# Optimization experiments

Measured on AMD Instinct MI355X. Metric: run time of the kernel, lower is better.

## Reference

```python
import jax, jax.numpy as jnp
import numpy as np

G, N, E, D, K = 32, 512, 8192, 256, 2048
LAMB_EDGE = 1.0
LAMB_NODE = 0.0
CODEBOOK_WEIGHT = 1000.0
ALPHA = 100.0


def setup_inputs() -> dict:
    key = jax.random.key(0)
    ks = jax.random.split(key, 12)
    s = 1.0 / np.sqrt(D)
    return {
        'feats': jax.random.normal(ks[0], (G, N, D), jnp.float32),
        'src': jax.random.randint(ks[1], (G, E), 0, N, jnp.int32),
        'dst': jax.random.randint(ks[2], (G, E), 0, N, jnp.int32),
        'W1': jax.random.normal(ks[3], (D, D), jnp.float32) * s,
        'b1': jnp.zeros((D,), jnp.float32),
        'W2': jax.random.normal(ks[4], (D, D), jnp.float32) * s,
        'b2': jnp.zeros((D,), jnp.float32),
        'ln_gamma': jnp.ones((D,), jnp.float32),
        'ln_beta': jnp.zeros((D,), jnp.float32),
        'dec1_W': jax.random.normal(ks[5], (D, D), jnp.float32) * s,
        'dec1_b': jnp.zeros((D,), jnp.float32),
        'dec2_W': jax.random.normal(ks[6], (D, D), jnp.float32) * s,
        'dec2_b': jnp.zeros((D,), jnp.float32),
        'codebook': jax.random.normal(ks[7], (K, D), jnp.float32),
    }


def _graph_conv(x, src, dst, W, b):
    # DGL GraphConv, norm='both': D_out^{-1/2} -> sum aggregate -> D_in^{-1/2} -> linear -> relu
    ones_e = jnp.ones(src.shape[0], x.dtype)
    deg_out = jnp.clip(jax.ops.segment_sum(ones_e, src, num_segments=N), 1.0)
    deg_in = jnp.clip(jax.ops.segment_sum(ones_e, dst, num_segments=N), 1.0)
    h = x * jax.lax.rsqrt(deg_out)[:, None]
    m = jax.ops.segment_sum(h[src], dst, num_segments=N)
    m = m * jax.lax.rsqrt(deg_in)[:, None]
    return jax.nn.relu(m @ W + b)


def _layernorm(x, gamma, beta):
    mu = jnp.mean(x, axis=-1, keepdims=True)
    var = jnp.mean(jnp.square(x - mu), axis=-1, keepdims=True)
    return (x - mu) * jax.lax.rsqrt(var + 1e-5) * gamma + beta


def _edge_loss(qe, src, dst):
    # qe: [N, D] decoded node embeddings for one graph
    logits = qe @ qe.T  # [N, N]
    adj = jnp.zeros((N, N), qe.dtype).at[src, dst].set(1.0)
    mask = jnp.triu(jnp.ones((N, N), bool), k=1)
    num_possible = N * N / 2.0
    num_edges = jnp.sum(jnp.where(mask, adj, 0.0))
    pos_weight = (num_possible - num_edges) / (num_edges + 1e-6)
    # BCEWithLogits with pos_weight, mean over strict upper triangle
    per = pos_weight * adj * jax.nn.softplus(-logits) + (1.0 - adj) * jax.nn.softplus(logits)
    return jnp.sum(jnp.where(mask, per, 0.0)) / (N * (N - 1) / 2.0)


def reference(feats, src, dst, W1, b1, W2, b2, ln_gamma, ln_beta,
              dec1_W, dec1_b, dec2_W, dec2_b, codebook):
    conv = jax.vmap(_graph_conv, in_axes=(0, 0, 0, None, None))
    h1 = conv(feats, src, dst, W1, b1)              # [G, N, D]
    h1 = _layernorm(h1, ln_gamma, ln_beta)           # dropout eval = identity
    h2 = conv(h1, src, dst, W2, b2)                  # [G, N, D]

    hf = h2.reshape(G * N, D)
    # cosine-sim VQ
    xn = hf * jax.lax.rsqrt(jnp.sum(hf * hf, -1, keepdims=True) + 1e-12)
    cn = codebook * jax.lax.rsqrt(jnp.sum(codebook * codebook, -1, keepdims=True) + 1e-12)
    dist = xn @ cn.T                                 # [G*N, K] cosine similarities
    idx = jnp.argmax(dist, axis=-1)
    q = codebook[idx]
    q_st = hf + jax.lax.stop_gradient(q - hf)        # straight-through
    vq_loss = CODEBOOK_WEIGHT * jnp.mean(jnp.square(q - jax.lax.stop_gradient(hf)))

    quantized_edge = (q_st @ dec1_W + dec1_b).reshape(G, N, D)
    quantized_node = q_st @ dec2_W + dec2_b

    edge_losses = jax.vmap(_edge_loss)(quantized_edge, src, dst)  # [G]
    edge_rec_loss = LAMB_EDGE * jnp.mean(edge_losses)
    feature_rec_loss = LAMB_NODE * jnp.mean(jnp.square(hf - quantized_node))
    loss = feature_rec_loss + edge_rec_loss * ALPHA + vq_loss
    return loss
```

## Files before the change

### kernel.cpp

```cpp
#include <hip/hip_runtime.h>
#include <math.h>

#define G 32
#define N 512
#define E 8192
#define D 256
#define KCB 2048
#define GN (G * N)

typedef __bf16 bf16x8 __attribute__((ext_vector_type(8)));
typedef float f32x4 __attribute__((ext_vector_type(4)));

static const size_t OFF_SPOS    = 0;
static const size_t OFF_SNEG    = OFF_SPOS + 256;
static const size_t OFF_NEDGE   = OFF_SNEG + 256;
static const size_t OFF_BEST    = OFF_NEDGE + 256;
static const size_t OFF_DEG_OUT = OFF_BEST + (size_t)GN * 8;
static const size_t OFF_DEG_IN  = OFF_DEG_OUT + (size_t)GN * 4;
static const size_t OFF_CURSOR  = OFF_DEG_IN + (size_t)GN * 4;
static const size_t OFF_ADJ     = OFF_CURSOR + (size_t)GN * 4;
static const size_t ZERO_BYTES  = OFF_ADJ + (size_t)G * N * N / 8;
static const size_t OFF_VQPART  = ZERO_BYTES;
static const size_t OFF_ROWOFF  = OFF_VQPART + (size_t)GN * 4;
static const size_t OFF_RS_OUT  = OFF_ROWOFF + (size_t)GN * 4;
static const size_t OFF_RS_IN   = OFF_RS_OUT + (size_t)GN * 4;
static const size_t OFF_CSR     = OFF_RS_IN + (size_t)GN * 4;
static const size_t OFF_RNC     = OFF_CSR + (size_t)G * E * 4;
static const size_t OFF_W1T     = OFF_RNC + (size_t)KCB * 4;
static const size_t OFF_W2T     = OFF_W1T + (size_t)D * D * 2;
static const size_t OFF_DWT     = OFF_W2T + (size_t)D * D * 2;
static const size_t OFF_CBB     = OFF_DWT + (size_t)D * D * 2;
static const size_t OFF_AGGB    = OFF_CBB + (size_t)KCB * D * 2;
static const size_t OFF_BF32    = OFF_AGGB + (size_t)GN * D * 2;
static const size_t OFF_BCB     = OFF_BF32 + (size_t)GN * D * 4;

__global__ void __launch_bounds__(256) k_build_deg(
    const int* __restrict__ src, const int* __restrict__ dst,
    int* __restrict__ deg_out, int* __restrict__ deg_in,
    unsigned* __restrict__ adj, int* __restrict__ nedge) {
  int b = blockIdx.x;
  int g = b >> 3;
  int e0 = (b & 7) << 10;
  int t = threadIdx.x;
  const int* sg = src + g * E;
  const int* dg = dst + g * E;
  int ecount = 0;
#pragma unroll
  for (int j = 0; j < 4; ++j) {
    int idx = e0 + j * 256 + t;
    int s = sg[idx], d = dg[idx];
    atomicAdd(&deg_out[(g << 9) | s], 1);
    atomicAdd(&deg_in[(g << 9) | d], 1);
    if (s < d) {
      int bit = s * N + d;
      unsigned m = 1u << (bit & 31);
      unsigned old = atomicOr(&adj[g * (N * N / 32) + (bit >> 5)], m);
      if (!(old & m)) ++ecount;
    }
  }
  for (int off = 32; off; off >>= 1) ecount += __shfl_down(ecount, off);
  __shared__ int sred[4];
  if ((t & 63) == 0) sred[t >> 6] = ecount;
  __syncthreads();
  if (t == 0) atomicAdd(&nedge[g], sred[0] + sred[1] + sred[2] + sred[3]);
}

__global__ void __launch_bounds__(512) k_build_scan(
    const int* __restrict__ deg_in, const int* __restrict__ deg_out,
    int* __restrict__ row_off, float* __restrict__ rs_in, float* __restrict__ rs_out) {
  int g = blockIdx.x, t = threadIdx.x;
  __shared__ int buf[2][N];
  int own = deg_in[(g << 9) | t];
  buf[0][t] = own;
  __syncthreads();
  int cur = 0;
  for (int off = 1; off < N; off <<= 1) {
    int v = buf[cur][t];
    if (t >= off) v += buf[cur][t - off];
    buf[cur ^ 1][t] = v;
    __syncthreads();
    cur ^= 1;
  }
  row_off[(g << 9) | t] = buf[cur][t] - own;
  rs_in[(g << 9) | t] = rsqrtf(fmaxf((float)own, 1.0f));
  rs_out[(g << 9) | t] = rsqrtf(fmaxf((float)deg_out[(g << 9) | t], 1.0f));
}

__global__ void __launch_bounds__(256) k_build_scatter(
    const int* __restrict__ src, const int* __restrict__ dst,
    const int* __restrict__ row_off, int* __restrict__ cursor, int* __restrict__ csr_src) {
  int b = blockIdx.x;
  int g = b >> 3;
  int e0 = (b & 7) << 10;
  int t = threadIdx.x;
  const int* sg = src + g * E;
  const int* dg = dst + g * E;
#pragma unroll
  for (int j = 0; j < 4; ++j) {
    int idx = e0 + j * 256 + t;
    int s = sg[idx], d = dg[idx];
    int gn = (g << 9) | d;
    int slot = atomicAdd(&cursor[gn], 1);
    csr_src[g * E + row_off[gn] + slot] = s;
  }
}

__global__ void __launch_bounds__(256) k_prep(
    const float* __restrict__ W1, const float* __restrict__ W2,
    const float* __restrict__ dW, __bf16* __restrict__ W1t,
    __bf16* __restrict__ W2t, __bf16* __restrict__ dWt,
    const float* __restrict__ cb, __bf16* __restrict__ cbb, float* __restrict__ rnc) {
  int b = blockIdx.x;
  if (b < 192) {
    __shared__ float tile[32][33];
    int z = b / 64, tt = b % 64;
    int bx = (tt & 7) * 32, by = (tt >> 3) * 32;
    const float* in = z == 0 ? W1 : (z == 1 ? W2 : dW);
    __bf16* out = z == 0 ? W1t : (z == 1 ? W2t : dWt);
    int tx = threadIdx.x & 31, ty = threadIdx.x >> 5;
#pragma unroll
    for (int r = 0; r < 32; r += 8) tile[ty + r][tx] = in[(by + ty + r) * D + bx + tx];
    __syncthreads();
#pragma unroll
    for (int r = 0; r < 32; r += 8)
      out[(size_t)(bx + ty + r) * D + by + tx] = (__bf16)tile[tx][ty + r];
  } else {
    int row = b - 192, t = threadIdx.x;
    float v = cb[(size_t)row * D + t];
    cbb[(size_t)row * D + t] = (__bf16)v;
    float s2 = v * v;
    for (int off = 32; off; off >>= 1) s2 += __shfl_down(s2, off);
    __shared__ float w[4];
    if ((t & 63) == 0) w[t >> 6] = s2;
    __syncthreads();
    if (t == 0) rnc[row] = rsqrtf(w[0] + w[1] + w[2] + w[3] + 1e-12f);
  }
}

template <bool FP32IN>
__global__ void __launch_bounds__(128) k_aggregate(
    const void* __restrict__ xin, const int* __restrict__ csr_src,
    const int* __restrict__ row_off, const int* __restrict__ deg_in,
    const float* __restrict__ rs_in, const float* __restrict__ rs_out,
    unsigned* __restrict__ out2) {
  int b = blockIdx.x;
  int g = ((b & 7) << 2) | (b >> 12);
  int n = (b >> 3) & 511;
  int gn = (g << 9) | n;
  int t = threadIdx.x;
  int cnt = deg_in[gn];
  int base = g * E + row_off[gn];
  __shared__ int sidx[128];
  __shared__ float sw[128];
  float ax = 0.f, ay = 0.f;
  for (int c0 = 0; c0 < cnt; c0 += 128) {
    int m = min(128, cnt - c0);
    if (t < m) {
      int s = csr_src[base + c0 + t];
      sidx[t] = s;
      sw[t] = rs_out[(g << 9) | s];
    }
    __syncthreads();
    for (int j = 0; j < m; ++j) {
      int s = sidx[j];
      float w = sw[j];
      size_t ridx = ((size_t)((g << 9) | s) << 7) + t;
      if (FP32IN) {
        float2 v = ((const float2*)xin)[ridx];
        ax += v.x * w;
        ay += v.y * w;
      } else {
        unsigned v = ((const unsigned*)xin)[ridx];
        ax += __uint_as_float(v << 16) * w;
        ay += __uint_as_float(v & 0xffff0000u) * w;
      }
    }
    __syncthreads();
  }
  float ri = rs_in[gn];
  union { __bf16 h[2]; unsigned u; } o;
  o.h[0] = (__bf16)(ax * ri);
  o.h[1] = (__bf16)(ay * ri);
  out2[((size_t)gn << 7) + t] = o.u;
}

__device__ __forceinline__ void gload_lds16(const __bf16* g, __bf16* s) {
  __builtin_amdgcn_global_load_lds((const __attribute__((address_space(1))) void*)g,
                                   (__attribute__((address_space(3))) void*)s, 16, 0, 0);
}

__device__ __forceinline__ void mfma_core(const __bf16* __restrict__ Abase,
                                          const __bf16* __restrict__ Bbase,
                                          __bf16* sA, __bf16* sB, f32x4 (&acc)[4][4],
                                          int tid) {
  int wave = tid >> 6, lane = tid & 63;
  int wr = (wave >> 1) * 64, wc = (wave & 1) * 64;
  int m = lane & 15, quad = lane >> 4;
  for (int k0 = 0; k0 < 256; k0 += 32) {
#pragma unroll
    for (int c2 = 0; c2 < 2; ++c2) {
      int c = wave * 2 + c2;
      int row = c * 16 + (lane >> 2);
      int col = (lane & 3) * 8;
      gload_lds16(Abase + (size_t)row * 256 + k0 + col, sA + c * 512);
      gload_lds16(Bbase + (size_t)row * 256 + k0 + col, sB + c * 512);
    }
    __syncthreads();
    bf16x8 af[4], bfr[4];
#pragma unroll
    for (int i = 0; i < 4; ++i) {
      af[i] = *(const bf16x8*)&sA[(wr + i * 16 + m) * 32 + quad * 8];
      bfr[i] = *(const bf16x8*)&sB[(wc + i * 16 + m) * 32 + quad * 8];
    }
#pragma unroll
    for (int i = 0; i < 4; ++i)
#pragma unroll
      for (int j = 0; j < 4; ++j)
        acc[i][j] = __builtin_amdgcn_mfma_f32_16x16x32_bf16(af[i], bfr[j], acc[i][j], 0, 0, 0);
    __syncthreads();
  }
}

template <bool RELU, bool SF32, bool SBF16>
__global__ void __launch_bounds__(256) k_gemm_bf16(
    const __bf16* __restrict__ A, const __bf16* __restrict__ Bt,
    const float* __restrict__ bias, float* __restrict__ C, __bf16* __restrict__ Cb) {
  __shared__ __align__(16) __bf16 sA[4096], sB[4096];
  f32x4 acc[4][4] = {};
  int tid = threadIdx.x;
  int row0 = blockIdx.x * 128, col0 = blockIdx.y * 128;
  mfma_core(A + (size_t)row0 * 256, Bt + (size_t)col0 * 256, sA, sB, acc, tid);
  int wave = tid >> 6, lane = tid & 63;
  int wr = (wave >> 1) * 64, wc = (wave & 1) * 64, quad = lane >> 4, n16 = lane & 15;
#pragma unroll
  for (int j = 0; j < 4; ++j) {
    int col = col0 + wc + j * 16 + n16;
    float bs = bias[col];
#pragma unroll
    for (int i = 0; i < 4; ++i)
#pragma unroll
      for (int r = 0; r < 4; ++r) {
        int row = row0 + wr + i * 16 + quad * 4 + r;
        float v = acc[i][j][r] + bs;
        if (RELU) v = fmaxf(v, 0.f);
        if (SF32) C[(size_t)row * 256 + col] = v;
        if (SBF16) Cb[(size_t)row * 256 + col] = (__bf16)v;
      }
  }
}

__global__ void __launch_bounds__(128) k_layernorm(
    unsigned* __restrict__ xb2, const float* __restrict__ gamma,
    const float* __restrict__ beta) {
  int row = blockIdx.x, t = threadIdx.x;
  unsigned u = xb2[row * 128 + t];
  float vx = __uint_as_float(u << 16), vy = __uint_as_float(u & 0xffff0000u);
  float s = vx + vy, s2 = vx * vx + vy * vy;
  for (int off = 32; off; off >>= 1) {
    s += __shfl_down(s, off);
    s2 += __shfl_down(s2, off);
  }
  __shared__ float w1[2], w2[2];
  if ((t & 63) == 0) { w1[t >> 6] = s; w2[t >> 6] = s2; }
  __syncthreads();
  float mu = (w1[0] + w1[1]) * (1.f / D);
  float m2 = (w2[0] + w2[1]) * (1.f / D);
  float rstd = rsqrtf(m2 - mu * mu + 1e-5f);
  float2 gm = ((const float2*)gamma)[t];
  float2 bt = ((const float2*)beta)[t];
  union { __bf16 h[2]; unsigned u; } o;
  o.h[0] = (__bf16)((vx - mu) * rstd * gm.x + bt.x);
  o.h[1] = (__bf16)((vy - mu) * rstd * gm.y + bt.y);
  xb2[row * 128 + t] = o.u;
}

__global__ void __launch_bounds__(256) k_vq_bf16(
    const __bf16* __restrict__ A, const __bf16* __restrict__ CBt,
    const float* __restrict__ rnc, unsigned long long* __restrict__ best) {
  __shared__ __align__(16) __bf16 sA[4096], sB[4096];
  f32x4 acc[4][4] = {};
  int tid = threadIdx.x;
  int row0 = blockIdx.x * 128, col0 = blockIdx.y * 128;
  mfma_core(A + (size_t)row0 * 256, CBt + (size_t)col0 * 256, sA, sB, acc, tid);
  int wave = tid >> 6, lane = tid & 63;
  int wr = (wave >> 1) * 64, wc = (wave & 1) * 64, quad = lane >> 4, n16 = lane & 15;
#pragma unroll
  for (int i = 0; i < 4; ++i) {
    unsigned long long cand[4] = {0ull, 0ull, 0ull, 0ull};
#pragma unroll
    for (int j = 0; j < 4; ++j) {
      int col = col0 + wc + j * 16 + n16;
      float rc = rnc[col];
#pragma unroll
      for (int r = 0; r < 4; ++r) {
        float sim = acc[i][j][r] * rc;
        unsigned u = __float_as_uint(sim);
        u = ((int)u >= 0) ? (u | 0x80000000u) : ~u;
        unsigned long long c64 =
            ((unsigned long long)u << 32) | (0xFFFFFFFFu - (unsigned)col);
        cand[r] = cand[r] > c64 ? cand[r] : c64;
      }
    }
#pragma unroll
    for (int off = 1; off < 16; off <<= 1)
#pragma unroll
      for (int r = 0; r < 4; ++r) {
        unsigned long long o = __shfl_xor(cand[r], off, 64);
        cand[r] = cand[r] > o ? cand[r] : o;
      }
    if (n16 == 0)
#pragma unroll
      for (int r = 0; r < 4; ++r)
        atomicMax(&best[row0 + wr + i * 16 + quad * 4 + r], cand[r]);
  }
}

__global__ void k_vq_gather(const unsigned long long* __restrict__ best,
                            const float* __restrict__ cb, const __bf16* __restrict__ cbb,
                            const float* __restrict__ hf, __bf16* __restrict__ qb,
                            float* __restrict__ vq_part) {
  int row = blockIdx.x, t = threadIdx.x;
  unsigned long long b = best[row];
  int c = (int)(0xFFFFFFFFu - (unsigned)(b & 0xFFFFFFFFull));
  qb[(size_t)row * D + t] = cbb[(size_t)c * D + t];
  float d = cb[(size_t)c * D + t] - hf[(size_t)row * D + t];
  float s2 = d * d;
  for (int off = 32; off; off >>= 1) s2 += __shfl_down(s2, off);
  __shared__ float w[4];
  if ((t & 63) == 0) w[t >> 6] = s2;
  __syncthreads();
  if (t == 0) vq_part[row] = w[0] + w[1] + w[2] + w[3];
}

__constant__ int c_ti[10] = {0, 0, 0, 0, 1, 1, 1, 2, 2, 3};
__constant__ int c_tj[10] = {0, 1, 2, 3, 1, 2, 3, 2, 3, 3};

__global__ void __launch_bounds__(256) k_edge_bf16(
    const __bf16* __restrict__ qe, const unsigned* __restrict__ adj,
    float* __restrict__ Spos, float* __restrict__ Sneg) {
  int g = blockIdx.x / 10, p = blockIdx.x % 10;
  int row0 = c_ti[p] * 128, col0 = c_tj[p] * 128;
  const __bf16* Ag = qe + (size_t)g * N * D;
  const unsigned* adjg = adj + (size_t)g * (N * N / 32);
  __shared__ __align__(16) __bf16 sA[4096], sB[4096];
  f32x4 acc[4][4] = {};
  int tid = threadIdx.x;
  mfma_core(Ag + (size_t)row0 * 256, Ag + (size_t)col0 * 256, sA, sB, acc, tid);
  int wave = tid >> 6, lane = tid & 63;
  int wr = (wave >> 1) * 64, wc = (wave & 1) * 64, quad = lane >> 4, n16 = lane & 15;
  float spos = 0.f, sneg = 0.f;
#pragma unroll
  for (int i = 0; i < 4; ++i)
#pragma unroll
    for (int j = 0; j < 4; ++j) {
      int c = col0 + wc + j * 16 + n16;
#pragma unroll
      for (int r = 0; r < 4; ++r) {
        int rr = row0 + wr + i * 16 + quad * 4 + r;
        if (rr < c) {
          float l = acc[i][j][r];
          int bit = rr * N + c;
          bool a = (adjg[bit >> 5] >> (bit & 31)) & 1u;
          float spabs = log1pf(expf(-fabsf(l)));
          if (a) spos += fmaxf(-l, 0.f) + spabs;
          else sneg += fmaxf(l, 0.f) + spabs;
        }
      }
    }
  for (int off = 32; off; off >>= 1) {
    spos += __shfl_down(spos, off);
    sneg += __shfl_down(sneg, off);
  }
  __shared__ float wp[4], wn[4];
  if ((tid & 63) == 0) { wp[tid >> 6] = spos; wn[tid >> 6] = sneg; }
  __syncthreads();
  if (tid == 0) {
    atomicAdd(&Spos[g], wp[0] + wp[1] + wp[2] + wp[3]);
    atomicAdd(&Sneg[g], wn[0] + wn[1] + wn[2] + wn[3]);
  }
}

__global__ void __launch_bounds__(256) k_final(
    const int* __restrict__ nedge, const float* __restrict__ Spos,
    const float* __restrict__ Sneg, const float* __restrict__ vq_part,
    float* __restrict__ out) {
  int t = threadIdx.x;
  float vq = 0.f;
  for (int i = t; i < GN; i += 256) vq += vq_part[i];
  float el = 0.f;
  if (t < G) {
    float ne = (float)nedge[t];
    float pw = (131072.0f - ne) / (ne + 1e-6f);
    el = (pw * Spos[t] + Sneg[t]) * (1.0f / 130816.0f);
  }
  for (int off = 32; off; off >>= 1) {
    vq += __shfl_down(vq, off);
    el += __shfl_down(el, off);
  }
  __shared__ float wv[4], we[4];
  if ((t & 63) == 0) { wv[t >> 6] = vq; we[t >> 6] = el; }
  __syncthreads();
  if (t == 0) {
    float vqs = wv[0] + wv[1] + wv[2] + wv[3];
    float els = we[0] + we[1] + we[2] + we[3];
    out[0] = 100.0f * (els * (1.0f / G)) + 1000.0f * (vqs * (1.0f / ((float)GN * D)));
  }
}

extern "C" void kernel_launch(void* const* d_in, const int* in_sizes, int n_in,
                              void* d_out, int out_size, void* d_ws, size_t ws_size,
                              hipStream_t stream) {
  const float* feats = (const float*)d_in[0];
  const int* src = (const int*)d_in[1];
  const int* dst = (const int*)d_in[2];
  const float* W1 = (const float*)d_in[3];
  const float* b1 = (const float*)d_in[4];
  const float* W2 = (const float*)d_in[5];
  const float* b2 = (const float*)d_in[6];
  const float* ln_g = (const float*)d_in[7];
  const float* ln_b = (const float*)d_in[8];
  const float* dec1_W = (const float*)d_in[9];
  const float* dec1_b = (const float*)d_in[10];
  const float* cb = (const float*)d_in[13];

  char* ws = (char*)d_ws;
  float* Spos = (float*)(ws + OFF_SPOS);
  float* Sneg = (float*)(ws + OFF_SNEG);
  int* nedge = (int*)(ws + OFF_NEDGE);
  unsigned long long* best = (unsigned long long*)(ws + OFF_BEST);
  int* deg_out = (int*)(ws + OFF_DEG_OUT);
  int* deg_in = (int*)(ws + OFF_DEG_IN);
  int* cursor = (int*)(ws + OFF_CURSOR);
  unsigned* adj = (unsigned*)(ws + OFF_ADJ);
  float* vq_part = (float*)(ws + OFF_VQPART);
  int* row_off = (int*)(ws + OFF_ROWOFF);
  float* rs_out = (float*)(ws + OFF_RS_OUT);
  float* rs_in = (float*)(ws + OFF_RS_IN);
  int* csr_src = (int*)(ws + OFF_CSR);
  float* rnc = (float*)(ws + OFF_RNC);
  __bf16* W1t = (__bf16*)(ws + OFF_W1T);
  __bf16* W2t = (__bf16*)(ws + OFF_W2T);
  __bf16* dWt = (__bf16*)(ws + OFF_DWT);
  __bf16* cbb = (__bf16*)(ws + OFF_CBB);
  __bf16* aggb = (__bf16*)(ws + OFF_AGGB);
  unsigned* aggb2 = (unsigned*)(ws + OFF_AGGB);
  float* bf32 = (float*)(ws + OFF_BF32);
  __bf16* bcb = (__bf16*)(ws + OFF_BCB);
  unsigned* bcb2 = (unsigned*)(ws + OFF_BCB);

  hipMemsetAsync(d_ws, 0, ZERO_BYTES, stream);

  k_build_deg<<<256, 256, 0, stream>>>(src, dst, deg_out, deg_in, adj, nedge);
  k_build_scan<<<G, 512, 0, stream>>>(deg_in, deg_out, row_off, rs_in, rs_out);
  k_build_scatter<<<256, 256, 0, stream>>>(src, dst, row_off, cursor, csr_src);
  k_prep<<<192 + KCB, 256, 0, stream>>>(W1, W2, dec1_W, W1t, W2t, dWt, cb, cbb, rnc);

  k_aggregate<true><<<GN, 128, 0, stream>>>(feats, csr_src, row_off, deg_in, rs_in,
                                            rs_out, aggb2);
  k_gemm_bf16<true, false, true><<<dim3(GN / 128, 2), 256, 0, stream>>>(
      aggb, W1t, b1, nullptr, bcb);
  k_layernorm<<<GN, 128, 0, stream>>>(bcb2, ln_g, ln_b);

  k_aggregate<false><<<GN, 128, 0, stream>>>(bcb2, csr_src, row_off, deg_in, rs_in,
                                             rs_out, aggb2);
  k_gemm_bf16<true, true, true><<<dim3(GN / 128, 2), 256, 0, stream>>>(
      aggb, W2t, b2, bf32, bcb);

  k_vq_bf16<<<dim3(GN / 128, KCB / 128), 256, 0, stream>>>(bcb, cbb, rnc, best);
  k_vq_gather<<<GN, 256, 0, stream>>>(best, cb, cbb, bf32, bcb, vq_part);

  k_gemm_bf16<false, false, true><<<dim3(GN / 128, 2), 256, 0, stream>>>(
      bcb, dWt, dec1_b, nullptr, aggb);
  k_edge_bf16<<<10 * G, 256, 0, stream>>>(aggb, adj, Spos, Sneg);

  k_final<<<1, 256, 0, stream>>>(nedge, Spos, Sneg, vq_part, (float*)d_out);
}
```

Measured before the change: 295.6 us.

## Replace CSR gather aggregation with dense normalized adjacency MFMA GEMM

Drops the CSR build (scan and scatter) and the per-node gather aggregation. Instead it builds a dense per-graph edge-count matrix, turns it into a bf16 adjacency matrix already scaled by both degree normalizations, transposes the features, and does the aggregation as a 512x512 by 512x256 MFMA GEMM per graph. This swaps irregular memory gathers for dense tensor-core work. In exchange it adds a 16 MB count matrix to zero every call, a 16 MB bf16 adjacency, transpose kernels, and extra rounding from storing the normalized adjacency in bf16.

```diff
diff --git a/kernel.cpp b/kernel.cpp
--- a/kernel.cpp
+++ b/kernel.cpp
@@ -11,37 +11,32 @@
 typedef __bf16 bf16x8 __attribute__((ext_vector_type(8)));
 typedef float f32x4 __attribute__((ext_vector_type(4)));
 
-static const size_t OFF_SPOS    = 0;
-static const size_t OFF_SNEG    = OFF_SPOS + 256;
-static const size_t OFF_NEDGE   = OFF_SNEG + 256;
-static const size_t OFF_BEST    = OFF_NEDGE + 256;
-static const size_t OFF_DEG_OUT = OFF_BEST + (size_t)GN * 8;
-static const size_t OFF_DEG_IN  = OFF_DEG_OUT + (size_t)GN * 4;
-static const size_t OFF_CURSOR  = OFF_DEG_IN + (size_t)GN * 4;
-static const size_t OFF_ADJ     = OFF_CURSOR + (size_t)GN * 4;
-static const size_t ZERO_BYTES  = OFF_ADJ + (size_t)G * N * N / 8;
-static const size_t OFF_VQPART  = ZERO_BYTES;
-static const size_t OFF_ROWOFF  = OFF_VQPART + (size_t)GN * 4;
-static const size_t OFF_RS_OUT  = OFF_ROWOFF + (size_t)GN * 4;
-static const size_t OFF_RS_IN   = OFF_RS_OUT + (size_t)GN * 4;
-static const size_t OFF_CSR     = OFF_RS_IN + (size_t)GN * 4;
-static const size_t OFF_RNC     = OFF_CSR + (size_t)G * E * 4;
-static const size_t OFF_W1T     = OFF_RNC + (size_t)KCB * 4;
-static const size_t OFF_W2T     = OFF_W1T + (size_t)D * D * 2;
-static const size_t OFF_DWT     = OFF_W2T + (size_t)D * D * 2;
-static const size_t OFF_CBB     = OFF_DWT + (size_t)D * D * 2;
-static const size_t OFF_AGGB    = OFF_CBB + (size_t)KCB * D * 2;
-static const size_t OFF_BF32    = OFF_AGGB + (size_t)GN * D * 2;
-static const size_t OFF_BCB     = OFF_BF32 + (size_t)GN * D * 4;
-
-__global__ void __launch_bounds__(256) k_build_deg(
+static const size_t OFF_SPOS   = 0;
+static const size_t OFF_SNEG   = OFF_SPOS + 256;
+static const size_t OFF_NEDGE  = OFF_SNEG + 256;
+static const size_t OFF_BEST   = OFF_NEDGE + 256;
+static const size_t OFF_DEGOUT = OFF_BEST + (size_t)GN * 8;
+static const size_t OFF_ADJ    = OFF_DEGOUT + (size_t)GN * 4;
+static const size_t OFF_CNT    = OFF_ADJ + (size_t)G * N * N / 8;
+static const size_t ZERO_BYTES = OFF_CNT + (size_t)G * N * N * 2;
+static const size_t OFF_DEGIN  = ZERO_BYTES;
+static const size_t OFF_VQPART = OFF_DEGIN + (size_t)GN * 4;
+static const size_t OFF_RNC    = OFF_VQPART + (size_t)GN * 4;
+static const size_t OFF_W1T    = OFF_RNC + (size_t)KCB * 4;
+static const size_t OFF_W2T    = OFF_W1T + (size_t)D * D * 2;
+static const size_t OFF_DWT    = OFF_W2T + (size_t)D * D * 2;
+static const size_t OFF_CBB    = OFF_DWT + (size_t)D * D * 2;
+static const size_t OFF_ABF    = OFF_CBB + (size_t)KCB * D * 2;
+static const size_t OFF_XT     = OFF_ABF + (size_t)G * N * N * 2;
+static const size_t OFF_AGGB   = OFF_XT + (size_t)G * D * N * 2;
+static const size_t OFF_BF32   = OFF_AGGB + (size_t)GN * D * 2;
+static const size_t OFF_BCB    = OFF_BF32 + (size_t)GN * D * 4;
+
+__global__ void __launch_bounds__(256) k_build_edges(
     const int* __restrict__ src, const int* __restrict__ dst,
-    int* __restrict__ deg_out, int* __restrict__ deg_in,
-    unsigned* __restrict__ adj, int* __restrict__ nedge) {
-  int b = blockIdx.x;
-  int g = b >> 3;
-  int e0 = (b & 7) << 10;
-  int t = threadIdx.x;
+    unsigned* __restrict__ cnt32, unsigned* __restrict__ adj, int* __restrict__ nedge) {
+  int b = blockIdx.x, t = threadIdx.x;
+  int g = b >> 3, e0 = (b & 7) << 10;
   const int* sg = src + g * E;
   const int* dg = dst + g * E;
   int ecount = 0;
@@ -49,8 +44,7 @@
   for (int j = 0; j < 4; ++j) {
     int idx = e0 + j * 256 + t;
     int s = sg[idx], d = dg[idx];
-    atomicAdd(&deg_out[(g << 9) | s], 1);
-    atomicAdd(&deg_in[(g << 9) | d], 1);
+    atomicAdd(&cnt32[g * (N * N / 2) + d * (N / 2) + (s >> 1)], 1u << ((s & 1) << 4));
     if (s < d) {
       int bit = s * N + d;
       unsigned m = 1u << (bit & 31);
@@ -65,43 +59,54 @@
   if (t == 0) atomicAdd(&nedge[g], sred[0] + sred[1] + sred[2] + sred[3]);
 }
 
-__global__ void __launch_bounds__(512) k_build_scan(
-    const int* __restrict__ deg_in, const int* __restrict__ deg_out,
-    int* __restrict__ row_off, float* __restrict__ rs_in, float* __restrict__ rs_out) {
-  int g = blockIdx.x, t = threadIdx.x;
-  __shared__ int buf[2][N];
-  int own = deg_in[(g << 9) | t];
-  buf[0][t] = own;
-  __syncthreads();
-  int cur = 0;
-  for (int off = 1; off < N; off <<= 1) {
-    int v = buf[cur][t];
-    if (t >= off) v += buf[cur][t - off];
-    buf[cur ^ 1][t] = v;
-    __syncthreads();
-    cur ^= 1;
-  }
-  row_off[(g << 9) | t] = buf[cur][t] - own;
-  rs_in[(g << 9) | t] = rsqrtf(fmaxf((float)own, 1.0f));
-  rs_out[(g << 9) | t] = rsqrtf(fmaxf((float)deg_out[(g << 9) | t], 1.0f));
-}
-
-__global__ void __launch_bounds__(256) k_build_scatter(
-    const int* __restrict__ src, const int* __restrict__ dst,
-    const int* __restrict__ row_off, int* __restrict__ cursor, int* __restrict__ csr_src) {
+__global__ void __launch_bounds__(256) k_sums(
+    const unsigned* __restrict__ cnt32, int* __restrict__ deg_in,
+    int* __restrict__ deg_out) {
   int b = blockIdx.x;
-  int g = b >> 3;
-  int e0 = (b & 7) << 10;
-  int t = threadIdx.x;
-  const int* sg = src + g * E;
-  const int* dg = dst + g * E;
-#pragma unroll
-  for (int j = 0; j < 4; ++j) {
-    int idx = e0 + j * 256 + t;
-    int s = sg[idx], d = dg[idx];
-    int gn = (g << 9) | d;
-    int slot = atomicAdd(&cursor[gn], 1);
-    csr_src[g * E + row_off[gn] + slot] = s;
+  int g = b >> 2, d0 = (b & 3) * 128;
+  int t = threadIdx.x, wave = t >> 6, lane = t & 63;
+  const unsigned* base = cnt32 + (size_t)g * (N * N / 2);
+  int clo[4] = {0, 0, 0, 0}, chi[4] = {0, 0, 0, 0};
+  for (int dd = 0; dd < 32; ++dd) {
+    int d = d0 + wave * 32 + dd;
+    int rs = 0;
+#pragma unroll
+    for (int c = 0; c < 4; ++c) {
+      unsigned v = base[d * (N / 2) + c * 64 + lane];
+      int lo = v & 0xffff, hi = v >> 16;
+      rs += lo + hi;
+      clo[c] += lo;
+      chi[c] += hi;
+    }
+    for (int off = 32; off; off >>= 1) rs += __shfl_down(rs, off);
+    if (lane == 0) deg_in[(g << 9) | d] = rs;
+  }
+#pragma unroll
+  for (int c = 0; c < 4; ++c) {
+    int s2 = (c * 64 + lane) * 2;
+    atomicAdd(&deg_out[(g << 9) | s2], clo[c]);
+    atomicAdd(&deg_out[(g << 9) | (s2 + 1)], chi[c]);
+  }
+}
+
+__global__ void __launch_bounds__(256) k_acast(
+    const unsigned* __restrict__ cnt32, const int* __restrict__ deg_in,
+    const int* __restrict__ deg_out, unsigned* __restrict__ abf2) {
+  int t = threadIdx.x, b = blockIdx.x;
+#pragma unroll
+  for (int q = 0; q < 4; ++q) {
+    int w = b * 1024 + q * 256 + t;
+    int g = w >> 17, d = (w >> 8) & 511, sp = w & 255;
+    unsigned v = cnt32[w];
+    float ri = rsqrtf(fmaxf((float)deg_in[(g << 9) | d], 1.f));
+    float a0 = (float)(v & 0xffff) * ri *
+               rsqrtf(fmaxf((float)deg_out[(g << 9) | (sp * 2)], 1.f));
+    float a1 = (float)(v >> 16) * ri *
+               rsqrtf(fmaxf((float)deg_out[(g << 9) | (sp * 2 + 1)], 1.f));
+    union { __bf16 h[2]; unsigned u; } o;
+    o.h[0] = (__bf16)a0;
+    o.h[1] = (__bf16)a1;
+    abf2[w] = o.u;
   }
 }
 
@@ -137,51 +142,20 @@
   }
 }
 
-template <bool FP32IN>
-__global__ void __launch_bounds__(128) k_aggregate(
-    const void* __restrict__ xin, const int* __restrict__ csr_src,
-    const int* __restrict__ row_off, const int* __restrict__ deg_in,
-    const float* __restrict__ rs_in, const float* __restrict__ rs_out,
-    unsigned* __restrict__ out2) {
+template <typename T>
+__global__ void __launch_bounds__(256) k_transpose(const T* __restrict__ in,
+                                                   __bf16* __restrict__ out) {
+  __shared__ __bf16 tile[64][66];
   int b = blockIdx.x;
-  int g = ((b & 7) << 2) | (b >> 12);
-  int n = (b >> 3) & 511;
-  int gn = (g << 9) | n;
-  int t = threadIdx.x;
-  int cnt = deg_in[gn];
-  int base = g * E + row_off[gn];
-  __shared__ int sidx[128];
-  __shared__ float sw[128];
-  float ax = 0.f, ay = 0.f;
-  for (int c0 = 0; c0 < cnt; c0 += 128) {
-    int m = min(128, cnt - c0);
-    if (t < m) {
-      int s = csr_src[base + c0 + t];
-      sidx[t] = s;
-      sw[t] = rs_out[(g << 9) | s];
-    }
-    __syncthreads();
-    for (int j = 0; j < m; ++j) {
-      int s = sidx[j];
-      float w = sw[j];
-      size_t ridx = ((size_t)((g << 9) | s) << 7) + t;
-      if (FP32IN) {
-        float2 v = ((const float2*)xin)[ridx];
-        ax += v.x * w;
-        ay += v.y * w;
-      } else {
-        unsigned v = ((const unsigned*)xin)[ridx];
-        ax += __uint_as_float(v << 16) * w;
-        ay += __uint_as_float(v & 0xffff0000u) * w;
-      }
-    }
-    __syncthreads();
-  }
-  float ri = rs_in[gn];
-  union { __bf16 h[2]; unsigned u; } o;
-  o.h[0] = (__bf16)(ax * ri);
-  o.h[1] = (__bf16)(ay * ri);
-  out2[((size_t)gn << 7) + t] = o.u;
+  int g = b >> 5, s0 = ((b >> 2) & 7) * 64, f0 = (b & 3) * 64;
+  int tx = threadIdx.x & 63, ty = threadIdx.x >> 6;
+#pragma unroll
+  for (int r = 0; r < 64; r += 4)
+    tile[ty + r][tx] = (__bf16)in[((size_t)(g * 512 + s0 + ty + r)) * 256 + f0 + tx];
+  __syncthreads();
+#pragma unroll
+  for (int r = 0; r < 64; r += 4)
+    out[(size_t)g * (D * N) + (size_t)(f0 + ty + r) * 512 + s0 + tx] = tile[tx][ty + r];
 }
 
 __device__ __forceinline__ void gload_lds16(const __bf16* g, __bf16* s) {
@@ -218,6 +192,58 @@
       for (int j = 0; j < 4; ++j)
         acc[i][j] = __builtin_amdgcn_mfma_f32_16x16x32_bf16(af[i], bfr[j], acc[i][j], 0, 0, 0);
     __syncthreads();
+  }
+}
+
+__global__ void __launch_bounds__(256) k_agg_mfma(
+    const __bf16* __restrict__ Abf, const __bf16* __restrict__ Xt,
+    __bf16* __restrict__ Mout) {
+  int b = blockIdx.x;
+  int xcd = b & 7, loc = b >> 3;
+  int g = (xcd << 2) | (loc >> 3);
+  int tile = loc & 7;
+  int row0 = (tile >> 1) * 128, col0 = (tile & 1) * 128;
+  const __bf16* Abase = Abf + (size_t)g * (N * N) + (size_t)row0 * 512;
+  const __bf16* Bbase = Xt + (size_t)g * (D * N) + (size_t)col0 * 512;
+  __shared__ __align__(16) __bf16 sA[4096], sB[4096];
+  f32x4 acc[4][4] = {};
+  int tid = threadIdx.x, wave = tid >> 6, lane = tid & 63;
+  int wr = (wave >> 1) * 64, wc = (wave & 1) * 64;
+  int m = lane & 15, quad = lane >> 4;
+  for (int k0 = 0; k0 < 512; k0 += 32) {
+#pragma unroll
+    for (int c2 = 0; c2 < 2; ++c2) {
+      int c = wave * 2 + c2;
+      int row = c * 16 + (lane >> 2);
+      int col = (lane & 3) * 8;
+      gload_lds16(Abase + (size_t)row * 512 + k0 + col, sA + c * 512);
+      gload_lds16(Bbase + (size_t)row * 512 + k0 + col, sB + c * 512);
+    }
+    __syncthreads();
+    bf16x8 af[4], bfr[4];
+#pragma unroll
+    for (int i = 0; i < 4; ++i) {
+      af[i] = *(const bf16x8*)&sA[(wr + i * 16 + m) * 32 + quad * 8];
+      bfr[i] = *(const bf16x8*)&sB[(wc + i * 16 + m) * 32 + quad * 8];
+    }
+#pragma unroll
+    for (int i = 0; i < 4; ++i)
+#pragma unroll
+      for (int j = 0; j < 4; ++j)
+        acc[i][j] = __builtin_amdgcn_mfma_f32_16x16x32_bf16(af[i], bfr[j], acc[i][j], 0, 0, 0);
+    __syncthreads();
+  }
+  int n16 = lane & 15;
+#pragma unroll
+  for (int j = 0; j < 4; ++j) {
+    int col = col0 + wc + j * 16 + n16;
+#pragma unroll
+    for (int i = 0; i < 4; ++i)
+#pragma unroll
+      for (int r = 0; r < 4; ++r) {
+        int row = (g << 9) + row0 + wr + i * 16 + quad * 4 + r;
+        Mout[(size_t)row * 256 + col] = (__bf16)acc[i][j][r];
+      }
   }
 }
 
@@ -428,41 +454,39 @@
   float* Sneg = (float*)(ws + OFF_SNEG);
   int* nedge = (int*)(ws + OFF_NEDGE);
   unsigned long long* best = (unsigned long long*)(ws + OFF_BEST);
-  int* deg_out = (int*)(ws + OFF_DEG_OUT);
-  int* deg_in = (int*)(ws + OFF_DEG_IN);
-  int* cursor = (int*)(ws + OFF_CURSOR);
+  int* deg_out = (int*)(ws + OFF_DEGOUT);
   unsigned* adj = (unsigned*)(ws + OFF_ADJ);
+  unsigned* cnt32 = (unsigned*)(ws + OFF_CNT);
+  int* deg_in = (int*)(ws + OFF_DEGIN);
   float* vq_part = (float*)(ws + OFF_VQPART);
-  int* row_off = (int*)(ws + OFF_ROWOFF);
-  float* rs_out = (float*)(ws + OFF_RS_OUT);
-  float* rs_in = (float*)(ws + OFF_RS_IN);
-  int* csr_src = (int*)(ws + OFF_CSR);
   float* rnc = (float*)(ws + OFF_RNC);
   __bf16* W1t = (__bf16*)(ws + OFF_W1T);
   __bf16* W2t = (__bf16*)(ws + OFF_W2T);
   __bf16* dWt = (__bf16*)(ws + OFF_DWT);
   __bf16* cbb = (__bf16*)(ws + OFF_CBB);
+  __bf16* abf = (__bf16*)(ws + OFF_ABF);
+  unsigned* abf2 = (unsigned*)(ws + OFF_ABF);
+  __bf16* xtb = (__bf16*)(ws + OFF_XT);
   __bf16* aggb = (__bf16*)(ws + OFF_AGGB);
-  unsigned* aggb2 = (unsigned*)(ws + OFF_AGGB);
   float* bf32 = (float*)(ws + OFF_BF32);
   __bf16* bcb = (__bf16*)(ws + OFF_BCB);
   unsigned* bcb2 = (unsigned*)(ws + OFF_BCB);
 
   hipMemsetAsync(d_ws, 0, ZERO_BYTES, stream);
 
-  k_build_deg<<<256, 256, 0, stream>>>(src, dst, deg_out, deg_in, adj, nedge);
-  k_build_scan<<<G, 512, 0, stream>>>(deg_in, deg_out, row_off, rs_in, rs_out);
-  k_build_scatter<<<256, 256, 0, stream>>>(src, dst, row_off, cursor, csr_src);
+  k_build_edges<<<256, 256, 0, stream>>>(src, dst, cnt32, adj, nedge);
+  k_sums<<<128, 256, 0, stream>>>(cnt32, deg_in, deg_out);
+  k_acast<<<4096, 256, 0, stream>>>(cnt32, deg_in, deg_out, abf2);
   k_prep<<<192 + KCB, 256, 0, stream>>>(W1, W2, dec1_W, W1t, W2t, dWt, cb, cbb, rnc);
-
-  k_aggregate<true><<<GN, 128, 0, stream>>>(feats, csr_src, row_off, deg_in, rs_in,
-                                            rs_out, aggb2);
+  k_transpose<float><<<1024, 256, 0, stream>>>(feats, xtb);
+
+  k_agg_mfma<<<256, 256, 0, stream>>>(abf, xtb, aggb);
   k_gemm_bf16<true, false, true><<<dim3(GN / 128, 2), 256, 0, stream>>>(
       aggb, W1t, b1, nullptr, bcb);
   k_layernorm<<<GN, 128, 0, stream>>>(bcb2, ln_g, ln_b);
 
-  k_aggregate<false><<<GN, 128, 0, stream>>>(bcb2, csr_src, row_off, deg_in, rs_in,
-                                             rs_out, aggb2);
+  k_transpose<__bf16><<<1024, 256, 0, stream>>>(bcb, xtb);
+  k_agg_mfma<<<256, 256, 0, stream>>>(abf, xtb, aggb);
   k_gemm_bf16<true, true, true><<<dim3(GN / 128, 2), 256, 0, stream>>>(
       aggb, W2t, b2, bf32, bcb);
 
```

After: 308.2 us. +4.3%, slower.
